# Optimization experiments

Hardware: AMD Instinct MI355X
Metric: run time of the kernel (lower is better)

## Reference

```python
import jax, jax.numpy as jnp
import numpy as np

EPS_ATTN = 1e-6
EPS_LN = 1e-5
NHEAD = 8


def _layernorm(x, g, b):
    mu = jnp.mean(x, axis=-1, keepdims=True)
    var = jnp.mean(jnp.square(x - mu), axis=-1, keepdims=True)
    return (x - mu) * jax.lax.rsqrt(var + EPS_LN) * g + b


def _feature_map(x):
    return jax.nn.elu(x) + 1.0


def setup_inputs() -> dict:
    key = jax.random.key(0)
    ks = jax.random.split(key, 8)
    N, L, S, C = 4, 8192, 8192, 256
    s = 1.0 / np.sqrt(C)
    return {
        "x": jax.random.normal(ks[0], (N, L, C), jnp.float32),
        "source": jax.random.normal(ks[1], (N, S, C), jnp.float32),
        "Wq": jax.random.normal(ks[2], (C, C), jnp.float32) * s,
        "Wk": jax.random.normal(ks[3], (C, C), jnp.float32) * s,
        "Wv": jax.random.normal(ks[4], (C, C), jnp.float32) * s,
        "Wmerge": jax.random.normal(ks[5], (C, C), jnp.float32) * s,
        "W1": jax.random.normal(ks[6], (2 * C, 2 * C), jnp.float32) * s,
        "W2": jax.random.normal(ks[7], (2 * C, C), jnp.float32) * s,
        "g1": jnp.ones((C,), jnp.float32),
        "b1": jnp.zeros((C,), jnp.float32),
        "g2": jnp.ones((C,), jnp.float32),
        "b2": jnp.zeros((C,), jnp.float32),
    }


def reference(x, source, Wq, Wk, Wv, Wmerge, W1, W2, g1, b1, g2, b2):
    N, L, C = x.shape
    S = source.shape[1]
    h, d = NHEAD, C // NHEAD

    q = (x @ Wq).reshape(N, L, h, d)
    k = (source @ Wk).reshape(N, S, h, d)
    v = (source @ Wv).reshape(N, S, h, d)

    Q = _feature_map(q)          # [N,L,h,d]
    K = _feature_map(k)          # [N,S,h,d]
    Vn = v / S                   # values / v_length

    KV = jnp.einsum('nshd,nshv->nhdv', K, Vn)             # [N,h,d,d]
    Ksum = K.sum(axis=1)                                  # [N,h,d]
    Z = 1.0 / (jnp.einsum('nlhd,nhd->nlh', Q, Ksum) + EPS_ATTN)
    msg = jnp.einsum('nlhd,nhdv,nlh->nlhv', Q, KV, Z) * S  # [N,L,h,d]

    msg = msg.reshape(N, L, C) @ Wmerge
    msg = _layernorm(msg, g1, b1)
    hcat = jnp.concatenate([x, msg], axis=2)              # [N,L,2C]
    msg = jax.nn.relu(hcat @ W1) @ W2
    msg = _layernorm(msg, g2, b2)
    return x + msg
```

## Files before the change

kernel.cpp:

```cpp
#include <hip/hip_runtime.h>
#include <hip/hip_bf16.h>
#include <stdint.h>

typedef __hip_bfloat16 bf16;
typedef __attribute__((ext_vector_type(8))) short short8;
typedef __attribute__((ext_vector_type(4))) short bf16x4;
typedef __attribute__((ext_vector_type(4))) float f32x4;

#define EPS_ATTN 1e-6f
#define EPS_LN   1e-5f

__device__ __forceinline__ float b2f(short s) {
    return __builtin_bit_cast(float, (unsigned)((unsigned short)s) << 16);
}
__device__ __forceinline__ short f2b(float f) {
    return __builtin_bit_cast(short, __float2bfloat16(f));
}

__device__ __forceinline__ void async16(const void* g, void* l) {
    __builtin_amdgcn_global_load_lds(
        (const __attribute__((address_space(1))) void*)g,
        (__attribute__((address_space(3))) void*)l,
        16, 0, 0);
}

__global__ __launch_bounds__(256)
void k_prep(const float* __restrict__ x, const float* __restrict__ src,
            bf16* __restrict__ x_bf, bf16* __restrict__ s_bf,
            const float* __restrict__ Wq, const float* __restrict__ Wk,
            const float* __restrict__ Wv, const float* __restrict__ Wm,
            const float* __restrict__ W1, const float* __restrict__ W2,
            bf16* __restrict__ WqT, bf16* __restrict__ WkT,
            bf16* __restrict__ WvT, bf16* __restrict__ WmT,
            bf16* __restrict__ W1T, bf16* __restrict__ W2T)
{
    __shared__ float tile[64][65];
    const int blk = blockIdx.x;
    if (blk < 8192) {
        const float* in = (blk < 4096) ? x : src;
        bf16* out       = (blk < 4096) ? x_bf : s_bf;
        const long id = (long)(blk & 4095) * 256 + threadIdx.x;
        const float4 a = ((const float4*)in)[id * 2];
        const float4 b = ((const float4*)in)[id * 2 + 1];
        short8 o;
        o[0] = f2b(a.x); o[1] = f2b(a.y); o[2] = f2b(a.z); o[3] = f2b(a.w);
        o[4] = f2b(b.x); o[5] = f2b(b.y); o[6] = f2b(b.z); o[7] = f2b(b.w);
        ((short8*)out)[id] = o;
        return;
    }
    const int b = blk - 8192;
    const float* W; bf16* WT; int K, N, local;
    if      (b < 16)  { W = Wq; WT = WqT; K = 256; N = 256; local = b; }
    else if (b < 32)  { W = Wk; WT = WkT; K = 256; N = 256; local = b - 16; }
    else if (b < 48)  { W = Wv; WT = WvT; K = 256; N = 256; local = b - 32; }
    else if (b < 64)  { W = Wm; WT = WmT; K = 256; N = 256; local = b - 48; }
    else if (b < 128) { W = W1; WT = W1T; K = 512; N = 512; local = b - 64; }
    else              { W = W2; WT = W2T; K = 512; N = 256; local = b - 128; }
    const int tk = K / 64;
    const int k0 = (local % tk) * 64, n0 = (local / tk) * 64;
    const int ty = threadIdx.x >> 4, tx = threadIdx.x & 15;
    #pragma unroll
    for (int i = 0; i < 4; ++i) {
        const int k = ty + i * 16;
        const float4 v = *(const float4*)&W[(long)(k0 + k) * N + n0 + tx * 4];
        tile[k][tx * 4 + 0] = v.x; tile[k][tx * 4 + 1] = v.y;
        tile[k][tx * 4 + 2] = v.z; tile[k][tx * 4 + 3] = v.w;
    }
    __syncthreads();
    #pragma unroll
    for (int i = 0; i < 4; ++i) {
        const int n = ty + i * 16;
        bf16x4 o;
        #pragma unroll
        for (int j = 0; j < 4; ++j) o[j] = f2b(tile[tx * 4 + j][n]);
        *(bf16x4*)&WT[(long)(n0 + n) * K + k0 + tx * 4] = o;
    }
}

__global__ __launch_bounds__(512)
void k_kvproj(const bf16* __restrict__ A, const bf16* __restrict__ BT,
              bf16* __restrict__ partKV, float* __restrict__ partKs,
              float escale)
{
    __shared__ __attribute__((aligned(16))) bf16 S[32768];
    bf16* Asm = S;
    bf16* Bsm = S + 8192;
    bf16* KT  = S;
    bf16* VT  = S + 16384;

    const int t = threadIdx.x, w = t >> 6, lane = t & 63;
    const int wm = w >> 2, wn = w & 3;
    const int flat = blockIdx.y * gridDim.x + blockIdx.x;
    const int swz  = (flat & 7) * 64 + (flat >> 3);
    const int cid  = swz >> 1;
    const int hh   = swz & 1;
    const long row0 = (long)cid * 128;
    const int lr = lane >> 3, lc = (lane & 7) * 8;
    const int lg = lane >> 4, l15 = lane & 15;

    f32x4 acc[4][4] = {};

    for (int kt = 0; kt < 256; kt += 64) {
        #pragma unroll
        for (int i = 0; i < 2; ++i) {
            const int g = w * 2 + i;
            async16(A + (row0 + g * 8 + lr) * 256 + kt + lc, &Asm[g * 512]);
        }
        #pragma unroll
        for (int i = 0; i < 4; ++i) {
            const int g = w * 4 + i;
            const long brow = (g < 16)
                ? (long)(hh * 128 + g * 8 + lr)
                : (long)(256 + hh * 128 + (g - 16) * 8 + lr);
            async16(BT + brow * 256 + kt + lc, &Bsm[g * 512]);
        }
        __syncthreads();
        #pragma unroll
        for (int ks = 0; ks < 2; ++ks) {
            short8 a[4], b[4];
            #pragma unroll
            for (int m = 0; m < 4; ++m)
                a[m] = *(const short8*)&Asm[(wm*64 + m*16 + l15)*64 + ks*32 + lg*8];
            #pragma unroll
            for (int n = 0; n < 4; ++n)
                b[n] = *(const short8*)&Bsm[(wn*64 + n*16 + l15)*64 + ks*32 + lg*8];
            #pragma unroll
            for (int m = 0; m < 4; ++m)
                #pragma unroll
                for (int n = 0; n < 4; ++n)
                    acc[m][n] = __builtin_amdgcn_mfma_f32_16x16x32_bf16(a[m], b[n], acc[m][n], 0, 0, 0);
        }
        __syncthreads();
    }

    const bool isK = wn < 2;
    bf16* tile = isK ? KT : VT;
    #pragma unroll
    for (int m = 0; m < 4; ++m) {
        #pragma unroll
        for (int n = 0; n < 4; ++n) {
            #pragma unroll
            for (int r = 0; r < 4; ++r) {
                const int row = wm * 64 + m * 16 + lg * 4 + r;
                const int col = (wn & 1) * 64 + n * 16 + l15;
                float v = acc[m][n][r];
                if (isK) v = v > 0.f ? v + 1.f : __expf(v);
                else     v *= escale;
                tile[row * 128 + col] = __float2bfloat16(v);
            }
        }
    }
    __syncthreads();

    const int h_l = t >> 7;
    const int d   = (t & 127) >> 2;
    const int vg  = t & 3;
    float a2[8] = {};
    float ks = 0.f;
    #pragma unroll 4
    for (int row = 0; row < 128; ++row) {
        const float kd = __bfloat162float(KT[row * 128 + h_l * 32 + d]);
        ks += kd;
        const short8 vv = *(const short8*)&VT[row * 128 + h_l * 32 + vg * 8];
        #pragma unroll
        for (int u = 0; u < 8; ++u) a2[u] += kd * b2f(vv[u]);
    }
    short8 o;
    #pragma unroll
    for (int u = 0; u < 8; ++u) o[u] = f2b(a2[u]);
    *(short8*)&partKV[(long)cid * 8192 + (hh * 4 + h_l) * 1024 + d * 32 + vg * 8] = o;
    if (vg == 0) partKs[cid * 256 + (hh * 4 + h_l) * 32 + d] = ks;
}

__global__ __launch_bounds__(256)
void k_kvred1(const bf16* __restrict__ partKV, const float* __restrict__ partKs,
              bf16* __restrict__ part2, float* __restrict__ part2Ks)
{
    const int bid = blockIdx.x;
    const int c8 = bid & 7, h = (bid >> 3) & 7, n = bid >> 6;
    const int t = threadIdx.x;
    const int d = t >> 3, vg = t & 7;
    float s[4] = {};
    #pragma unroll
    for (int j = 0; j < 8; ++j) {
        const int cid = n * 64 + c8 * 8 + j;
        const bf16x4 p = *(const bf16x4*)&partKV[(long)cid * 8192 + h * 1024 + d * 32 + vg * 4];
        #pragma unroll
        for (int jj = 0; jj < 4; ++jj) s[jj] += b2f(p[jj]);
    }
    bf16x4 o;
    #pragma unroll
    for (int jj = 0; jj < 4; ++jj) o[jj] = f2b(s[jj]);
    *(bf16x4*)&part2[(long)(c8 * 4 + n) * 8192 + h * 1024 + d * 32 + vg * 4] = o;
    if (vg == 0) {
        float ks = 0.f;
        #pragma unroll
        for (int j = 0; j < 8; ++j) {
            const int cid = n * 64 + c8 * 8 + j;
            ks += partKs[cid * 256 + h * 32 + d];
        }
        part2Ks[(c8 * 4 + n) * 256 + h * 32 + d] = ks;
    }
}

__global__ __launch_bounds__(256)
void k_kvred2(const bf16* __restrict__ part2, const float* __restrict__ part2Ks,
              bf16* __restrict__ KVb)
{
    const int b = blockIdx.x;
    const int n = b >> 3, h = b & 7;
    const int t = threadIdx.x;
    const int d = t >> 3, vg = t & 7;
    float s[4] = {};
    #pragma unroll
    for (int c8 = 0; c8 < 8; ++c8) {
        const bf16x4 p = *(const bf16x4*)&part2[(long)(c8 * 4 + n) * 8192 + h * 1024 + d * 32 + vg * 4];
        #pragma unroll
        for (int j = 0; j < 4; ++j) s[j] += b2f(p[j]);
    }
    bf16* dst = KVb + ((long)n * 8 + h) * 1536 + d * 48;
    bf16x4 o;
    #pragma unroll
    for (int j = 0; j < 4; ++j) o[j] = f2b(s[j]);
    *(bf16x4*)&dst[vg * 4] = o;
    if (vg == 0) {
        float ks = 0.f;
        #pragma unroll
        for (int c8 = 0; c8 < 8; ++c8) ks += part2Ks[(c8 * 4 + n) * 256 + h * 32 + d];
        short8 z0 = {};
        z0[0] = f2b(ks);
        *(short8*)&dst[32] = z0;
        short8 zz = {};
        *(short8*)&dst[40] = zz;
    }
}

__global__ __launch_bounds__(512)
void k_qaml(const bf16* __restrict__ xb, const bf16* __restrict__ WqT,
            const bf16* __restrict__ WmT, const bf16* __restrict__ KVb,
            const float* __restrict__ g, const float* __restrict__ b,
            bf16* __restrict__ msgln)
{
    __shared__ __attribute__((aligned(16))) bf16 Asm[64 * 64];
    __shared__ __attribute__((aligned(16))) bf16 Bsm[256 * 64];
    __shared__ __attribute__((aligned(16))) bf16 QM[64 * 264];
    __shared__ float lnS[4][64];
    __shared__ float lnQ[4][64];
    const int t = threadIdx.x, w = t >> 6, lane = t & 63;
    const int wm = w >> 2, wn = w & 3;
    const long row0 = (long)blockIdx.x * 64;
    const int n_b = (int)(row0 >> 13);
    const int lr = lane >> 3, lc = (lane & 7) * 8;
    const int lg = lane >> 4, l15 = lane & 15;

    {
        f32x4 acc[2][4] = {};
        for (int kt = 0; kt < 256; kt += 64) {
            async16(xb + (row0 + w * 8 + lr) * 256 + kt + lc, &Asm[w * 512]);
            #pragma unroll
            for (int i = 0; i < 4; ++i) {
                const int ch = i * 8 + w;
                async16(WqT + (long)(ch * 8 + lr) * 256 + kt + lc, &Bsm[ch * 512]);
            }
            __syncthreads();
            #pragma unroll
            for (int ks = 0; ks < 2; ++ks) {
                short8 a[2], bb[4];
                #pragma unroll
                for (int m = 0; m < 2; ++m)
                    a[m] = *(const short8*)&Asm[(wm*32 + m*16 + l15)*64 + ks*32 + lg*8];
                #pragma unroll
                for (int n = 0; n < 4; ++n)
                    bb[n] = *(const short8*)&Bsm[(wn*64 + n*16 + l15)*64 + ks*32 + lg*8];
                #pragma unroll
                for (int m = 0; m < 2; ++m)
                    #pragma unroll
                    for (int n = 0; n < 4; ++n)
                        acc[m][n] = __builtin_amdgcn_mfma_f32_16x16x32_bf16(a[m], bb[n], acc[m][n], 0, 0, 0);
            }
            __syncthreads();
        }
        #pragma unroll
        for (int m = 0; m < 2; ++m) {
            #pragma unroll
            for (int n = 0; n < 4; ++n) {
                #pragma unroll
                for (int r = 0; r < 4; ++r) {
                    const int row = wm * 32 + m * 16 + lg * 4 + r;
                    const int col = wn * 64 + n * 16 + l15;
                    float v = acc[m][n][r];
                    v = v > 0.f ? v + 1.f : __expf(v);
                    QM[row * 264 + col] = __float2bfloat16(v);
                }
            }
        }
    }
    __syncthreads();

    {
        const bf16* kvh = KVb + (long)n_b * 12288 + w * 1536;
        short8 b0, b1, bz;
        #pragma unroll
        for (int j = 0; j < 8; ++j) {
            const int drow = (lg * 8 + j) * 48;
            b0[j] = __builtin_bit_cast(short, kvh[drow + l15]);
            b1[j] = __builtin_bit_cast(short, kvh[drow + 16 + l15]);
            bz[j] = __builtin_bit_cast(short, kvh[drow + 32 + l15]);
        }
        f32x4 ra0[4], ra1[4];
        #pragma unroll
        for (int m2 = 0; m2 < 4; ++m2) {
            const short8 a = *(const short8*)&QM[(m2 * 16 + l15) * 264 + w * 32 + lg * 8];
            f32x4 a0 = {}, a1 = {}, az = {};
            a0 = __builtin_amdgcn_mfma_f32_16x16x32_bf16(a, b0, a0, 0, 0, 0);
            a1 = __builtin_amdgcn_mfma_f32_16x16x32_bf16(a, b1, a1, 0, 0, 0);
            az = __builtin_amdgcn_mfma_f32_16x16x32_bf16(a, bz, az, 0, 0, 0);
            #pragma unroll
            for (int r = 0; r < 4; ++r) {
                const float z   = __shfl(az[r], lane & 48);
                const float inv = 8192.f / (z + EPS_ATTN);
                ra0[m2][r] = a0[r] * inv;
                ra1[m2][r] = a1[r] * inv;
            }
        }
        __syncthreads();
        #pragma unroll
        for (int m2 = 0; m2 < 4; ++m2) {
            #pragma unroll
            for (int r = 0; r < 4; ++r) {
                const int row = m2 * 16 + lg * 4 + r;
                QM[row * 264 + w * 32 + l15]      = __float2bfloat16(ra0[m2][r]);
                QM[row * 264 + w * 32 + 16 + l15] = __float2bfloat16(ra1[m2][r]);
            }
        }
    }
    __syncthreads();

    f32x4 acc[2][4] = {};
    for (int kt = 0; kt < 256; kt += 64) {
        #pragma unroll
        for (int i = 0; i < 4; ++i) {
            const int ch = i * 8 + w;
            async16(WmT + (long)(ch * 8 + lr) * 256 + kt + lc, &Bsm[ch * 512]);
        }
        __syncthreads();
        #pragma unroll
        for (int ks = 0; ks < 2; ++ks) {
            short8 a[2], bb[4];
            #pragma unroll
            for (int m = 0; m < 2; ++m)
                a[m] = *(const short8*)&QM[(wm*32 + m*16 + l15) * 264 + kt + ks*32 + lg*8];
            #pragma unroll
            for (int n = 0; n < 4; ++n)
                bb[n] = *(const short8*)&Bsm[(wn*64 + n*16 + l15)*64 + ks*32 + lg*8];
            #pragma unroll
            for (int m = 0; m < 2; ++m)
                #pragma unroll
                for (int n = 0; n < 4; ++n)
                    acc[m][n] = __builtin_amdgcn_mfma_f32_16x16x32_bf16(a[m], bb[n], acc[m][n], 0, 0, 0);
        }
        __syncthreads();
    }

    #pragma unroll
    for (int m = 0; m < 2; ++m) {
        #pragma unroll
        for (int r = 0; r < 4; ++r) {
            float ls = 0.f, lq = 0.f;
            #pragma unroll
            for (int n = 0; n < 4; ++n) {
                const float v = acc[m][n][r];
                ls += v; lq += v * v;
            }
            #pragma unroll
            for (int o = 1; o < 16; o <<= 1) {
                ls += __shfl_xor(ls, o);
                lq += __shfl_xor(lq, o);
            }
            if (l15 == 0) {
                const int row = wm * 32 + m * 16 + lg * 4 + r;
                lnS[wn][row] = ls;
                lnQ[wn][row] = lq;
            }
        }
    }
    __syncthreads();

    float gv[4], bv[4];
    #pragma unroll
    for (int n = 0; n < 4; ++n) {
        const int col = wn * 64 + n * 16 + l15;
        gv[n] = g[col]; bv[n] = b[col];
    }
    #pragma unroll
    for (int m = 0; m < 2; ++m) {
        #pragma unroll
        for (int r = 0; r < 4; ++r) {
            const int row = wm * 32 + m * 16 + lg * 4 + r;
            const float S  = lnS[0][row] + lnS[1][row] + lnS[2][row] + lnS[3][row];
            const float Qq = lnQ[0][row] + lnQ[1][row] + lnQ[2][row] + lnQ[3][row];
            const float mean = S * (1.f / 256.f);
            const float var  = Qq * (1.f / 256.f) - mean * mean;
            const float rstd = rsqrtf(var + EPS_LN);
            const long grow = row0 + row;
            #pragma unroll
            for (int n = 0; n < 4; ++n) {
                const int col = wn * 64 + n * 16 + l15;
                const float y = (acc[m][n][r] - mean) * rstd * gv[n] + bv[n];
                msgln[grow * 256 + col] = __float2bfloat16(y);
            }
        }
    }
}

__global__ __launch_bounds__(512, 2)
void k_gemmW1_8p(const bf16* __restrict__ A0, const bf16* __restrict__ A1,
                 const bf16* __restrict__ BT, bf16* __restrict__ C)
{
    __shared__ __attribute__((aligned(16))) bf16 S[65536];
    const int t = threadIdx.x, w = t >> 6, lane = t & 63;
    const int wm = w >> 2, wn = w & 3;
    const int lg = lane >> 4, l15 = lane & 15;
    const int orig = blockIdx.y * gridDim.x + blockIdx.x;
    const int swz  = (orig & 7) * 32 + (orig >> 3);
    const long row0 = (long)(swz >> 1) * 256;
    const long col0 = (long)(swz & 1) * 256;

    f32x4 acc[8][4] = {};
    short8 av[4], bv0[4], bv1[4];

    auto stageA = [&](int tile, int half) {
        if (tile >= 8) return;
        const bf16* Asrc = (tile < 4) ? A0 : A1;
        const int kbase = (tile & 3) * 64;
        #pragma unroll
        for (int i = 0; i < 2; ++i) {
            const int cbase = i * 512 + w * 64;
            const int c = cbase + lane;
            const int srow = c >> 3;
            const int lcol = 8 * ((c & 7) ^ (srow & 7));
            async16(Asrc + (row0 + half * 128 + srow) * 256 + kbase + lcol,
                    &S[(tile & 1) * 32768 + half * 8192 + cbase * 8]);
        }
    };
    auto stageB = [&](int tile, int half) {
        if (tile >= 8) return;
        const int kbase = tile * 64;
        #pragma unroll
        for (int i = 0; i < 2; ++i) {
            const int cbase = i * 512 + w * 64;
            const int c = cbase + lane;
            const int srow = c >> 3;
            const int lcol = 8 * ((c & 7) ^ (srow & 7));
            async16(BT + (col0 + half * 128 + srow) * 512 + kbase + lcol,
                    &S[(tile & 1) * 32768 + 16384 + half * 8192 + cbase * 8]);
        }
    };

#define RD_A(BUF, MH, KS) do { _Pragma("unroll")                               \
    for (int m_ = 0; m_ < 4; ++m_) {                                           \
        const int row_ = wm * 128 + (MH) * 64 + m_ * 16 + l15;                 \
        av[m_] = *(const short8*)&S[(BUF) * 32768 + row_ * 64 +                \
                 (((KS) * 32 + lg * 8) ^ ((row_ & 7) << 3))]; } } while (0)

#define RD_B(BUF, KS, BV) do { _Pragma("unroll")                               \
    for (int n_ = 0; n_ < 4; ++n_) {                                           \
        const int row_ = wn * 64 + n_ * 16 + l15;                              \
        (BV)[n_] = *(const short8*)&S[(BUF) * 32768 + 16384 + row_ * 64 +      \
                 (((KS) * 32 + lg * 8) ^ ((row_ & 7) << 3))]; } } while (0)

#define DO_MFMA(MH, BV) do { __builtin_amdgcn_s_setprio(1); _Pragma("unroll")  \
    for (int m_ = 0; m_ < 4; ++m_) { _Pragma("unroll")                         \
        for (int n_ = 0; n_ < 4; ++n_)                                         \
            acc[(MH) * 4 + m_][n_] = __builtin_amdgcn_mfma_f32_16x16x32_bf16(  \
                av[m_], (BV)[n_], acc[(MH) * 4 + m_][n_], 0, 0, 0); }          \
    __builtin_amdgcn_s_setprio(0); } while (0)

#define BAR() __builtin_amdgcn_s_barrier()

    stageB(0, 0); stageB(0, 1); stageA(0, 0); stageA(0, 1);
    stageB(1, 0); stageB(1, 1);
    asm volatile("s_waitcnt vmcnt(4)" ::: "memory");
    BAR();

    for (int it = 0; it < 4; ++it) {
        const int T1 = 2 * it + 1;
        RD_B(0, 0, bv0); RD_A(0, 0, 0); stageA(T1, 0);
        BAR(); DO_MFMA(0, bv0); BAR();
        RD_B(0, 1, bv1); RD_A(0, 0, 1); stageA(T1, 1);
        BAR(); DO_MFMA(0, bv1); BAR();
        RD_A(0, 1, 0); stageB(T1 + 1, 0);
        BAR(); DO_MFMA(1, bv0); BAR();
        RD_A(0, 1, 1); stageB(T1 + 1, 1);
        BAR(); DO_MFMA(1, bv1);
        if (it == 3) asm volatile("s_waitcnt vmcnt(0)" ::: "memory");
        else         asm volatile("s_waitcnt vmcnt(4)" ::: "memory");
        BAR();
        RD_B(1, 0, bv0); RD_A(1, 0, 0); stageA(T1 + 1, 0);
        BAR(); DO_MFMA(0, bv0); BAR();
        RD_B(1, 1, bv1); RD_A(1, 0, 1); stageA(T1 + 1, 1);
        BAR(); DO_MFMA(0, bv1); BAR();
        RD_A(1, 1, 0); stageB(T1 + 2, 0);
        BAR(); DO_MFMA(1, bv0); BAR();
        RD_A(1, 1, 1); stageB(T1 + 2, 1);
        BAR(); DO_MFMA(1, bv1);
        if (it < 3) asm volatile("s_waitcnt vmcnt(4)" ::: "memory");
        BAR();
    }

    #pragma unroll
    for (int mi = 0; mi < 8; ++mi) {
        #pragma unroll
        for (int n = 0; n < 4; ++n) {
            #pragma unroll
            for (int r = 0; r < 4; ++r) {
                const long row = row0 + wm * 128 + mi * 16 + lg * 4 + r;
                const long col = col0 + wn * 64 + n * 16 + l15;
                const float v = acc[mi][n][r];
                C[row * 512 + col] = __float2bfloat16(v > 0.f ? v : 0.f);
            }
        }
    }
#undef RD_A
#undef RD_B
#undef DO_MFMA
#undef BAR
}

__global__ __launch_bounds__(512)
void k_gemm_ln2(const bf16* __restrict__ A, const bf16* __restrict__ BT,
                const float* __restrict__ g, const float* __restrict__ b,
                const float* __restrict__ xres, float* __restrict__ out)
{
    __shared__ __attribute__((aligned(16))) bf16 Asm[64 * 64];
    __shared__ __attribute__((aligned(16))) bf16 Bsm[256 * 64];
    __shared__ float lnS[4][64];
    __shared__ float lnQ[4][64];
    const int t = threadIdx.x, w = t >> 6, lane = t & 63;
    const int wm = w >> 2, wn = w & 3;
    const long row0 = (long)blockIdx.x * 64;
    const int lr = lane >> 3, lc = (lane & 7) * 8;
    const int lg = lane >> 4, l15 = lane & 15;

    f32x4 acc[2][4] = {};

    for (int kt = 0; kt < 512; kt += 64) {
        async16(A + (row0 + w * 8 + lr) * 512 + kt + lc, &Asm[w * 512]);
        #pragma unroll
        for (int i = 0; i < 4; ++i) {
            const int ch = i * 8 + w;
            async16(BT + (long)(ch * 8 + lr) * 512 + kt + lc, &Bsm[ch * 512]);
        }
        __syncthreads();
        #pragma unroll
        for (int ks = 0; ks < 2; ++ks) {
            short8 a[2], bb[4];
            #pragma unroll
            for (int m = 0; m < 2; ++m)
                a[m] = *(const short8*)&Asm[(wm*32 + m*16 + l15)*64 + ks*32 + lg*8];
            #pragma unroll
            for (int n = 0; n < 4; ++n)
                bb[n] = *(const short8*)&Bsm[(wn*64 + n*16 + l15)*64 + ks*32 + lg*8];
            #pragma unroll
            for (int m = 0; m < 2; ++m)
                #pragma unroll
                for (int n = 0; n < 4; ++n)
                    acc[m][n] = __builtin_amdgcn_mfma_f32_16x16x32_bf16(a[m], bb[n], acc[m][n], 0, 0, 0);
        }
        __syncthreads();
    }

    #pragma unroll
    for (int m = 0; m < 2; ++m) {
        #pragma unroll
        for (int r = 0; r < 4; ++r) {
            float ls = 0.f, lq = 0.f;
            #pragma unroll
            for (int n = 0; n < 4; ++n) {
                const float v = acc[m][n][r];
                ls += v; lq += v * v;
            }
            #pragma unroll
            for (int o = 1; o < 16; o <<= 1) {
                ls += __shfl_xor(ls, o);
                lq += __shfl_xor(lq, o);
            }
            if (l15 == 0) {
                const int row = wm * 32 + m * 16 + lg * 4 + r;
                lnS[wn][row] = ls;
                lnQ[wn][row] = lq;
            }
        }
    }
    __syncthreads();

    float gv[4], bv[4];
    #pragma unroll
    for (int n = 0; n < 4; ++n) {
        const int col = wn * 64 + n * 16 + l15;
        gv[n] = g[col]; bv[n] = b[col];
    }
    #pragma unroll
    for (int m = 0; m < 2; ++m) {
        #pragma unroll
        for (int r = 0; r < 4; ++r) {
            const int row = wm * 32 + m * 16 + lg * 4 + r;
            const float S  = lnS[0][row] + lnS[1][row] + lnS[2][row] + lnS[3][row];
            const float Qq = lnQ[0][row] + lnQ[1][row] + lnQ[2][row] + lnQ[3][row];
            const float mean = S * (1.f / 256.f);
            const float var  = Qq * (1.f / 256.f) - mean * mean;
            const float rstd = rsqrtf(var + EPS_LN);
            const long grow = row0 + row;
            #pragma unroll
            for (int n = 0; n < 4; ++n) {
                const int col = wn * 64 + n * 16 + l15;
                const float y = (acc[m][n][r] - mean) * rstd * gv[n] + bv[n];
                out[grow * 256 + col] = xres[grow * 256 + col] + y;
            }
        }
    }
}

extern "C" void kernel_launch(void* const* d_in, const int* in_sizes, int n_in,
                              void* d_out, int out_size, void* d_ws, size_t ws_size,
                              hipStream_t stream)
{
    const float* x      = (const float*)d_in[0];
    const float* source = (const float*)d_in[1];
    const float* Wq     = (const float*)d_in[2];
    const float* Wk     = (const float*)d_in[3];
    const float* Wv     = (const float*)d_in[4];
    const float* Wm     = (const float*)d_in[5];
    const float* W1     = (const float*)d_in[6];
    const float* W2     = (const float*)d_in[7];
    const float* g1     = (const float*)d_in[8];
    const float* b1     = (const float*)d_in[9];
    const float* g2     = (const float*)d_in[10];
    const float* b2     = (const float*)d_in[11];
    float* out = (float*)d_out;

    const size_t U = 32768ull * 256ull;
    char* w = (char*)d_ws;

    bf16* x_bf  = (bf16*)(w + 0 * U * 2);
    bf16* s_bf  = (bf16*)(w + 1 * U * 2);
    bf16* msgln = (bf16*)(w + 2 * U * 2);
    bf16* t_bf  = (bf16*)(w + 3 * U * 2);

    char* wx = w + 7 * U * 2;
    bf16* WqT = (bf16*)wx; wx += 65536 * 2;
    bf16* WkT = (bf16*)wx; wx += 65536 * 2;
    bf16* WvT = (bf16*)wx; wx += 65536 * 2;
    bf16* WmT = (bf16*)wx; wx += 65536 * 2;
    bf16* W1T = (bf16*)wx; wx += 262144 * 2;
    bf16* W2T = (bf16*)wx; wx += 131072 * 2;
    bf16* partKV = (bf16*)wx; wx += 2097152 * 2;
    float* partKs = (float*)wx; wx += 65536 * 4;
    bf16* part2  = (bf16*)wx; wx += 262144 * 2;
    float* part2Ks = (float*)wx; wx += 8192 * 4;
    bf16* KVb    = (bf16*)wx; wx += 49152 * 2;

    const dim3 blk(256);

    k_prep<<<8352, blk, 0, stream>>>(x, source, x_bf, s_bf,
                                     Wq, Wk, Wv, Wm, W1, W2,
                                     WqT, WkT, WvT, WmT, W1T, W2T);

    k_kvproj<<<dim3(256, 2), dim3(512), 0, stream>>>(s_bf, WkT, partKV, partKs,
                                                     1.f / 8192.f);

    k_kvred1<<<256, blk, 0, stream>>>(partKV, partKs, part2, part2Ks);
    k_kvred2<<<32, blk, 0, stream>>>(part2, part2Ks, KVb);

    k_qaml<<<512, dim3(512), 0, stream>>>(x_bf, WqT, WmT, KVb, g1, b1, msgln);

    k_gemmW1_8p<<<dim3(128, 2), dim3(512), 0, stream>>>(x_bf, msgln, W1T, t_bf);
    k_gemm_ln2<<<512, dim3(512), 0, stream>>>(t_bf, W2T, g2, b2, x, out);
}
```

Measured before the change: 131.4 us.

## Rewrite W2+LayerNorm GEMM as 256-row 8-phase pipelined kernel with swizzled LDS

Replaces the 64-row-per-block W2 GEMM with a 256x256 tile kernel. It double-buffers A and B tiles in an XOR-swizzled 128KB LDS array and interleaves async loads with MFMA phases separated by barriers and priority hints. Block indices are remapped, and the LayerNorm reduction buffers reuse the staging LDS. The intent is to cut redundant B loads, bank conflicts and load stalls. In exchange the grid shrinks to 128 blocks, each needing high register and LDS use, which may underfill the GPU's CUs.

```diff
diff --git a/kernel.cpp b/kernel.cpp
--- a/kernel.cpp
+++ b/kernel.cpp
@@ -527,57 +527,112 @@
 #undef BAR
 }
 
-__global__ __launch_bounds__(512)
-void k_gemm_ln2(const bf16* __restrict__ A, const bf16* __restrict__ BT,
-                const float* __restrict__ g, const float* __restrict__ b,
-                const float* __restrict__ xres, float* __restrict__ out)
+__global__ __launch_bounds__(512, 2)
+void k_ln2_8p(const bf16* __restrict__ A, const bf16* __restrict__ BT,
+              const float* __restrict__ g, const float* __restrict__ b,
+              const float* __restrict__ xres, float* __restrict__ out)
 {
-    __shared__ __attribute__((aligned(16))) bf16 Asm[64 * 64];
-    __shared__ __attribute__((aligned(16))) bf16 Bsm[256 * 64];
-    __shared__ float lnS[4][64];
-    __shared__ float lnQ[4][64];
+    __shared__ __attribute__((aligned(16))) bf16 S[65536];
     const int t = threadIdx.x, w = t >> 6, lane = t & 63;
     const int wm = w >> 2, wn = w & 3;
-    const long row0 = (long)blockIdx.x * 64;
-    const int lr = lane >> 3, lc = (lane & 7) * 8;
     const int lg = lane >> 4, l15 = lane & 15;
-
-    f32x4 acc[2][4] = {};
-
-    for (int kt = 0; kt < 512; kt += 64) {
-        async16(A + (row0 + w * 8 + lr) * 512 + kt + lc, &Asm[w * 512]);
-        #pragma unroll
-        for (int i = 0; i < 4; ++i) {
-            const int ch = i * 8 + w;
-            async16(BT + (long)(ch * 8 + lr) * 512 + kt + lc, &Bsm[ch * 512]);
-        }
-        __syncthreads();
-        #pragma unroll
-        for (int ks = 0; ks < 2; ++ks) {
-            short8 a[2], bb[4];
-            #pragma unroll
-            for (int m = 0; m < 2; ++m)
-                a[m] = *(const short8*)&Asm[(wm*32 + m*16 + l15)*64 + ks*32 + lg*8];
-            #pragma unroll
-            for (int n = 0; n < 4; ++n)
-                bb[n] = *(const short8*)&Bsm[(wn*64 + n*16 + l15)*64 + ks*32 + lg*8];
-            #pragma unroll
-            for (int m = 0; m < 2; ++m)
-                #pragma unroll
-                for (int n = 0; n < 4; ++n)
-                    acc[m][n] = __builtin_amdgcn_mfma_f32_16x16x32_bf16(a[m], bb[n], acc[m][n], 0, 0, 0);
-        }
-        __syncthreads();
-    }
-
-    #pragma unroll
-    for (int m = 0; m < 2; ++m) {
+    const int orig = blockIdx.x;
+    const int swz  = (orig & 7) * 16 + (orig >> 3);
+    const long row0 = (long)swz * 256;
+
+    f32x4 acc[8][4] = {};
+    short8 av[4], bv0[4], bv1[4];
+
+    auto stageA = [&](int tile, int half) {
+        if (tile >= 8) return;
+        const int kbase = tile * 64;
+        #pragma unroll
+        for (int i = 0; i < 2; ++i) {
+            const int cbase = i * 512 + w * 64;
+            const int c = cbase + lane;
+            const int srow = c >> 3;
+            const int lcol = 8 * ((c & 7) ^ (srow & 7));
+            async16(A + (row0 + half * 128 + srow) * 512 + kbase + lcol,
+                    &S[(tile & 1) * 32768 + half * 8192 + cbase * 8]);
+        }
+    };
+    auto stageB = [&](int tile, int half) {
+        if (tile >= 8) return;
+        const int kbase = tile * 64;
+        #pragma unroll
+        for (int i = 0; i < 2; ++i) {
+            const int cbase = i * 512 + w * 64;
+            const int c = cbase + lane;
+            const int srow = c >> 3;
+            const int lcol = 8 * ((c & 7) ^ (srow & 7));
+            async16(BT + (long)(half * 128 + srow) * 512 + kbase + lcol,
+                    &S[(tile & 1) * 32768 + 16384 + half * 8192 + cbase * 8]);
+        }
+    };
+
+#define RD_A(BUF, MH, KS) do { _Pragma("unroll")                               \
+    for (int m_ = 0; m_ < 4; ++m_) {                                           \
+        const int row_ = wm * 128 + (MH) * 64 + m_ * 16 + l15;                 \
+        av[m_] = *(const short8*)&S[(BUF) * 32768 + row_ * 64 +                \
+                 (((KS) * 32 + lg * 8) ^ ((row_ & 7) << 3))]; } } while (0)
+
+#define RD_B(BUF, KS, BV) do { _Pragma("unroll")                               \
+    for (int n_ = 0; n_ < 4; ++n_) {                                           \
+        const int row_ = wn * 64 + n_ * 16 + l15;                              \
+        (BV)[n_] = *(const short8*)&S[(BUF) * 32768 + 16384 + row_ * 64 +      \
+                 (((KS) * 32 + lg * 8) ^ ((row_ & 7) << 3))]; } } while (0)
+
+#define DO_MFMA(MH, BV) do { __builtin_amdgcn_s_setprio(1); _Pragma("unroll")  \
+    for (int m_ = 0; m_ < 4; ++m_) { _Pragma("unroll")                         \
+        for (int n_ = 0; n_ < 4; ++n_)                                         \
+            acc[(MH) * 4 + m_][n_] = __builtin_amdgcn_mfma_f32_16x16x32_bf16(  \
+                av[m_], (BV)[n_], acc[(MH) * 4 + m_][n_], 0, 0, 0); }          \
+    __builtin_amdgcn_s_setprio(0); } while (0)
+
+#define BAR() __builtin_amdgcn_s_barrier()
+
+    stageB(0, 0); stageB(0, 1); stageA(0, 0); stageA(0, 1);
+    stageB(1, 0); stageB(1, 1);
+    asm volatile("s_waitcnt vmcnt(4)" ::: "memory");
+    BAR();
+
+    for (int it = 0; it < 4; ++it) {
+        const int T1 = 2 * it + 1;
+        RD_B(0, 0, bv0); RD_A(0, 0, 0); stageA(T1, 0);
+        BAR(); DO_MFMA(0, bv0); BAR();
+        RD_B(0, 1, bv1); RD_A(0, 0, 1); stageA(T1, 1);
+        BAR(); DO_MFMA(0, bv1); BAR();
+        RD_A(0, 1, 0); stageB(T1 + 1, 0);
+        BAR(); DO_MFMA(1, bv0); BAR();
+        RD_A(0, 1, 1); stageB(T1 + 1, 1);
+        BAR(); DO_MFMA(1, bv1);
+        if (it == 3) asm volatile("s_waitcnt vmcnt(0)" ::: "memory");
+        else         asm volatile("s_waitcnt vmcnt(4)" ::: "memory");
+        BAR();
+        RD_B(1, 0, bv0); RD_A(1, 0, 0); stageA(T1 + 1, 0);
+        BAR(); DO_MFMA(0, bv0); BAR();
+        RD_B(1, 1, bv1); RD_A(1, 0, 1); stageA(T1 + 1, 1);
+        BAR(); DO_MFMA(0, bv1); BAR();
+        RD_A(1, 1, 0); stageB(T1 + 2, 0);
+        BAR(); DO_MFMA(1, bv0); BAR();
+        RD_A(1, 1, 1); stageB(T1 + 2, 1);
+        BAR(); DO_MFMA(1, bv1);
+        if (it < 3) asm volatile("s_waitcnt vmcnt(4)" ::: "memory");
+        BAR();
+    }
+
+    __syncthreads();
+    float* lnS = (float*)S;
+    float* lnQ = (float*)((char*)S + 4096);
+
+    #pragma unroll
+    for (int mi = 0; mi < 8; ++mi) {
         #pragma unroll
         for (int r = 0; r < 4; ++r) {
             float ls = 0.f, lq = 0.f;
             #pragma unroll
             for (int n = 0; n < 4; ++n) {
-                const float v = acc[m][n][r];
+                const float v = acc[mi][n][r];
                 ls += v; lq += v * v;
             }
             #pragma unroll
@@ -586,9 +641,9 @@
                 lq += __shfl_xor(lq, o);
             }
             if (l15 == 0) {
-                const int row = wm * 32 + m * 16 + lg * 4 + r;
-                lnS[wn][row] = ls;
-                lnQ[wn][row] = lq;
+                const int row = wm * 128 + mi * 16 + lg * 4 + r;
+                lnS[wn * 256 + row] = ls;
+                lnQ[wn * 256 + row] = lq;
             }
         }
     }
@@ -601,24 +656,28 @@
         gv[n] = g[col]; bv[n] = b[col];
     }
     #pragma unroll
-    for (int m = 0; m < 2; ++m) {
+    for (int mi = 0; mi < 8; ++mi) {
         #pragma unroll
         for (int r = 0; r < 4; ++r) {
-            const int row = wm * 32 + m * 16 + lg * 4 + r;
-            const float S  = lnS[0][row] + lnS[1][row] + lnS[2][row] + lnS[3][row];
-            const float Qq = lnQ[0][row] + lnQ[1][row] + lnQ[2][row] + lnQ[3][row];
-            const float mean = S * (1.f / 256.f);
+            const int row = wm * 128 + mi * 16 + lg * 4 + r;
+            const float Sm = lnS[row] + lnS[256 + row] + lnS[512 + row] + lnS[768 + row];
+            const float Qq = lnQ[row] + lnQ[256 + row] + lnQ[512 + row] + lnQ[768 + row];
+            const float mean = Sm * (1.f / 256.f);
             const float var  = Qq * (1.f / 256.f) - mean * mean;
             const float rstd = rsqrtf(var + EPS_LN);
             const long grow = row0 + row;
             #pragma unroll
             for (int n = 0; n < 4; ++n) {
                 const int col = wn * 64 + n * 16 + l15;
-                const float y = (acc[m][n][r] - mean) * rstd * gv[n] + bv[n];
+                const float y = (acc[mi][n][r] - mean) * rstd * gv[n] + bv[n];
                 out[grow * 256 + col] = xres[grow * 256 + col] + y;
             }
         }
     }
+#undef RD_A
+#undef RD_B
+#undef DO_MFMA
+#undef BAR
 }
 
 extern "C" void kernel_launch(void* const* d_in, const int* in_sizes, int n_in,
@@ -675,5 +734,5 @@
     k_qaml<<<512, dim3(512), 0, stream>>>(x_bf, WqT, WmT, KVb, g1, b1, msgln);
 
     k_gemmW1_8p<<<dim3(128, 2), dim3(512), 0, stream>>>(x_bf, msgln, W1T, t_bf);
-    k_gemm_ln2<<<512, dim3(512), 0, stream>>>(t_bf, W2T, g2, b2, x, out);
-}
+    k_ln2_8p<<<128, dim3(512), 0, stream>>>(t_bf, W2T, g2, b2, x, out);
+}
```

Result: no change. 131.3 us (-0.1%).
